# Kernel optimization log

Measured on AMD Instinct MI355X. Metric: run time of the kernel, lower is better.

## Reference

```python
import jax, jax.numpy as jnp
import numpy as np

D_MODEL = 512
NHEAD = 8
HEAD_DIM = D_MODEL // NHEAD
NS = 1  # num_special_tokens


def setup_inputs() -> dict:
    key = jax.random.key(0)
    ks = jax.random.split(key, 12)
    B, N = 8, 1024
    x = jax.random.normal(ks[0], (B, N, D_MODEL), dtype=jnp.float32)
    coords = jax.random.normal(ks[1], (B, N, 3), dtype=jnp.float32) * 5.0
    key_padding_mask = jnp.zeros((B, N), dtype=bool)
    s = 1.0 / np.sqrt(D_MODEL)
    qkv_w = jax.random.normal(ks[2], (3 * D_MODEL, D_MODEL), dtype=jnp.float32) * s
    out_w = jax.random.normal(ks[3], (D_MODEL, D_MODEL), dtype=jnp.float32) * s
    out_b = jnp.zeros((D_MODEL,), dtype=jnp.float32)
    bias_alpha = jnp.ones((1,), dtype=jnp.float32) * 0.5  # nonzero so bias path matters
    w1 = jax.random.normal(ks[4], (NHEAD * 4, 4), dtype=jnp.float32) * 0.5
    b1 = jnp.zeros((NHEAD * 4,), dtype=jnp.float32)
    w2 = jax.random.normal(ks[5], (NHEAD, NHEAD * 4), dtype=jnp.float32) * 0.2
    b2 = jnp.zeros((NHEAD,), dtype=jnp.float32)
    coord_scales = jnp.array([12.0, 12.0, 5.0], dtype=jnp.float32)
    return dict(x=x, coords=coords, key_padding_mask=key_padding_mask,
                qkv_w=qkv_w, out_w=out_w, out_b=out_b, bias_alpha=bias_alpha,
                w1=w1, b1=b1, w2=w2, b2=b2, coord_scales=coord_scales)


def reference(x, coords, key_padding_mask, qkv_w, out_w, out_b, bias_alpha,
              w1, b1, w2, b2, coord_scales):
    B, N, _ = x.shape
    scale = HEAD_DIM ** (-0.5)
    qkv = x @ qkv_w.T  # [B,N,3D]
    q, k, v = jnp.split(qkv, 3, axis=-1)
    def heads(t):
        return t.reshape(B, N, NHEAD, HEAD_DIM).transpose(0, 2, 1, 3)  # [B,H,N,dh]
    q, k, v = heads(q), heads(k), heads(v)

    c = coords / coord_scales  # [B,N,3]
    dpos = c[:, :, None, :] - c[:, None, :, :]  # [B,N,N,3]
    dist = jnp.linalg.norm(dpos, axis=-1, keepdims=True)  # [B,N,N,1]
    feat = jnp.concatenate([dpos, dist], axis=-1)  # [B,N,N,4]
    h = jax.nn.gelu(feat @ w1.T + b1, approximate=False)  # [B,N,N,4H]
    bias = (h @ w2.T + b2).transpose(0, 3, 1, 2)  # [B,H,N,N]
    # zero out bias rows/cols for special tokens
    bias = bias.at[:, :, :NS, :].set(0.0)
    bias = bias.at[:, :, :, :NS].set(0.0)

    dots = jnp.einsum('bhid,bhjd->bhij', q, k) * scale
    logits = dots + bias_alpha * bias
    logits = jnp.where(key_padding_mask[:, None, None, :], -1e30, logits)
    attn = jax.nn.softmax(logits, axis=-1)
    out = jnp.einsum('bhij,bhjd->bhid', attn, v)
    out = out.transpose(0, 2, 1, 3).reshape(B, N, D_MODEL)
    return out @ out_w.T + out_b
```

## Files before the change

### kernel.cpp

```cpp
#include <hip/hip_runtime.h>
#include <hip/hip_bf16.h>
#include <math.h>

#define D_MODEL 512
#define NHEAD   8
#define HEAD_DIM 64
#define BB      8
#define NN      1024
#define NS      1
#define TI      16
#define TJ      32
#define NT      (NN / TJ)
#define FIX_M   10.0f
#define GSTRIDE 40

typedef __attribute__((ext_vector_type(8))) short short8;
typedef __attribute__((ext_vector_type(4))) float floatx4;

__device__ __forceinline__ float gelu_tanh(float x) {
    const float x2 = x * x;
    const float z  = x * fmaf(0.0713548162f, x2, 1.5957691216f);
    const float e  = __expf(z);
    const float r  = __builtin_amdgcn_rcpf(1.0f + e);
    return fmaf(-x, r, x);
}

__device__ __forceinline__ unsigned short f2bf(float f) {
    unsigned u = __float_as_uint(f);
    u = (u + 0x7fffu + ((u >> 16) & 1u)) >> 16;
    return (unsigned short)u;
}

__device__ __forceinline__ uint2 pack4bf(float a, float b, float c, float d) {
    uint2 p;
    p.x = (unsigned)f2bf(a) | ((unsigned)f2bf(b) << 16);
    p.y = (unsigned)f2bf(c) | ((unsigned)f2bf(d) << 16);
    return p;
}

__global__ __launch_bounds__(256)
void gemm_qkv_mfma(const float* __restrict__ A, const float* __restrict__ Bm,
                   unsigned short* __restrict__ Qb, unsigned short* __restrict__ Kb,
                   unsigned short* __restrict__ Vt) {
    __shared__ __align__(16) unsigned short As[128 * GSTRIDE];
    __shared__ __align__(16) unsigned short Bs[128 * GSTRIDE];
    const int tid = threadIdx.x;
    const int bm = blockIdx.y * 128;
    const int bn = blockIdx.x * 128;
    const int wv = tid >> 6, lane = tid & 63, quad = lane >> 4, ln = lane & 15;
    const int wm = (wv >> 1) * 64, wn = (wv & 1) * 64;

    floatx4 acc[4][4];
    #pragma unroll
    for (int i = 0; i < 4; ++i)
        #pragma unroll
        for (int j = 0; j < 4; ++j) acc[i][j] = (floatx4){0.f, 0.f, 0.f, 0.f};

    for (int k0 = 0; k0 < 512; k0 += 32) {
        __syncthreads();
        #pragma unroll
        for (int t = 0; t < 4; ++t) {
            const int c = tid + t * 256;
            const int row = c >> 3, kc = (c & 7) * 4;
            float4 v = *(const float4*)(A + (size_t)(bm + row) * 512 + k0 + kc);
            *(uint2*)&As[row * GSTRIDE + kc] = pack4bf(v.x, v.y, v.z, v.w);
            float4 w = *(const float4*)(Bm + (size_t)(bn + row) * 512 + k0 + kc);
            *(uint2*)&Bs[row * GSTRIDE + kc] = pack4bf(w.x, w.y, w.z, w.w);
        }
        __syncthreads();
        short8 af[4], bf[4];
        #pragma unroll
        for (int mb = 0; mb < 4; ++mb)
            af[mb] = *(const short8*)&As[(wm + mb * 16 + ln) * GSTRIDE + quad * 8];
        #pragma unroll
        for (int nb = 0; nb < 4; ++nb)
            bf[nb] = *(const short8*)&Bs[(wn + nb * 16 + ln) * GSTRIDE + quad * 8];
        #pragma unroll
        for (int mb = 0; mb < 4; ++mb)
            #pragma unroll
            for (int nb = 0; nb < 4; ++nb)
                acc[mb][nb] = __builtin_amdgcn_mfma_f32_16x16x32_bf16(af[mb], bf[nb], acc[mb][nb], 0, 0, 0);
    }

    #pragma unroll
    for (int nb = 0; nb < 4; ++nb) {
        const int n = bn + wn + nb * 16 + ln;
        #pragma unroll
        for (int mb = 0; mb < 4; ++mb) {
            const int m = bm + wm + mb * 16 + quad * 4;
            if (n < 512) {
                #pragma unroll
                for (int r = 0; r < 4; ++r)
                    Qb[(size_t)(m + r) * 512 + n] = f2bf(acc[mb][nb][r] * 0.125f);
            } else if (n < 1024) {
                #pragma unroll
                for (int r = 0; r < 4; ++r)
                    Kb[(size_t)(m + r) * 512 + (n - 512)] = f2bf(acc[mb][nb][r]);
            } else {
                const int bb = m >> 10, tok = m & 1023;
                *(uint2*)(Vt + ((size_t)bb * 512 + (n - 1024)) * NN + tok) =
                    pack4bf(acc[mb][nb][0], acc[mb][nb][1], acc[mb][nb][2], acc[mb][nb][3]);
            }
        }
    }
}

__global__ __launch_bounds__(256)
void gemm_out_mfma(const unsigned short* __restrict__ Ab, const float* __restrict__ Bm,
                   const float* __restrict__ bias, float* __restrict__ C) {
    __shared__ __align__(16) unsigned short As[128 * GSTRIDE];
    __shared__ __align__(16) unsigned short Bs[128 * GSTRIDE];
    const int tid = threadIdx.x;
    const int bm = blockIdx.y * 128;
    const int bn = blockIdx.x * 128;
    const int wv = tid >> 6, lane = tid & 63, quad = lane >> 4, ln = lane & 15;
    const int wm = (wv >> 1) * 64, wn = (wv & 1) * 64;

    floatx4 acc[4][4];
    #pragma unroll
    for (int i = 0; i < 4; ++i)
        #pragma unroll
        for (int j = 0; j < 4; ++j) acc[i][j] = (floatx4){0.f, 0.f, 0.f, 0.f};

    for (int k0 = 0; k0 < 512; k0 += 32) {
        __syncthreads();
        #pragma unroll
        for (int t = 0; t < 4; ++t) {
            const int c = tid + t * 256;
            const int row = c >> 3, kc = (c & 7) * 4;
            *(uint2*)&As[row * GSTRIDE + kc] =
                *(const uint2*)(Ab + (size_t)(bm + row) * 512 + k0 + kc);
            float4 w = *(const float4*)(Bm + (size_t)(bn + row) * 512 + k0 + kc);
            *(uint2*)&Bs[row * GSTRIDE + kc] = pack4bf(w.x, w.y, w.z, w.w);
        }
        __syncthreads();
        short8 af[4], bf[4];
        #pragma unroll
        for (int mb = 0; mb < 4; ++mb)
            af[mb] = *(const short8*)&As[(wm + mb * 16 + ln) * GSTRIDE + quad * 8];
        #pragma unroll
        for (int nb = 0; nb < 4; ++nb)
            bf[nb] = *(const short8*)&Bs[(wn + nb * 16 + ln) * GSTRIDE + quad * 8];
        #pragma unroll
        for (int mb = 0; mb < 4; ++mb)
            #pragma unroll
            for (int nb = 0; nb < 4; ++nb)
                acc[mb][nb] = __builtin_amdgcn_mfma_f32_16x16x32_bf16(af[mb], bf[nb], acc[mb][nb], 0, 0, 0);
    }

    #pragma unroll
    for (int nb = 0; nb < 4; ++nb) {
        const int n = bn + wn + nb * 16 + ln;
        const float bv = bias[n];
        #pragma unroll
        for (int mb = 0; mb < 4; ++mb) {
            const int m = bm + wm + mb * 16 + quad * 4;
            #pragma unroll
            for (int r = 0; r < 4; ++r)
                C[(size_t)(m + r) * 512 + n] = acc[mb][nb][r] + bv;
        }
    }
}

#define BIAS_IDX(i, j, h) ((i) * 291 + (j) * 9 + (h))
__global__ __launch_bounds__(256, 2)
void attn_kernel(const unsigned short* __restrict__ Qb,
                 const unsigned short* __restrict__ Kb,
                 const unsigned short* __restrict__ Vt,
                 const float* __restrict__ coords,
                 const unsigned char* __restrict__ mask,
                 const float* __restrict__ w1, const float* __restrict__ b1,
                 const float* __restrict__ w2, const float* __restrict__ b2,
                 const float* __restrict__ coord_scales,
                 const float* __restrict__ alpha_p,
                 unsigned short* __restrict__ attn_out) {
    const int b   = blockIdx.y;
    const int i0  = blockIdx.x * TI;
    const int tid = threadIdx.x;
    const int wv  = tid >> 6;
    const int lane = tid & 63;
    const int quad = lane >> 4;
    const int ln   = lane & 15;
    const int h0   = wv * 2;

    __shared__ float bias_s[2][TI * 291 + 9];
    __shared__ __align__(16) unsigned short ps[NHEAD][TI][40];

    const float alpha = alpha_p[0];
    const float isx = 1.0f / coord_scales[0];
    const float isy = 1.0f / coord_scales[1];
    const float isz = 1.0f / coord_scales[2];

    float cir[4][3];
    #pragma unroll
    for (int g = 0; g < 4; ++g) {
        const float* cp = coords + ((size_t)b * NN + i0 + wv * 4 + g) * 3;
        cir[g][0] = cp[0] * isx; cir[g][1] = cp[1] * isy; cir[g][2] = cp[2] * isz;
    }

    float4 w1r[8]; float b1r[8];
    #pragma unroll
    for (int jj = 0; jj < 8; ++jj) {
        w1r[jj] = *(const float4*)(w1 + (quad * 8 + jj) * 4);
        b1r[jj] = b1[quad * 8 + jj];
    }
    short8 b2f;
    #pragma unroll
    for (int jj = 0; jj < 8; ++jj) {
        const float v = (ln < 8) ? alpha * w2[ln * 32 + quad * 8 + jj] : 0.0f;
        b2f[jj] = (short)f2bf(v);
    }
    const float ab2 = (ln < 8) ? alpha * b2[ln] : 0.0f;

    short8 qf[2][2];
    #pragma unroll
    for (int hh = 0; hh < 2; ++hh)
        #pragma unroll
        for (int kd = 0; kd < 2; ++kd)
            qf[hh][kd] = *(const short8*)(Qb + ((size_t)b * NN + i0 + ln) * 512
                                          + (h0 + hh) * 64 + kd * 32 + quad * 8);

    floatx4 oacc[2][4];
    #pragma unroll
    for (int hh = 0; hh < 2; ++hh)
        #pragma unroll
        for (int nd = 0; nd < 4; ++nd)
            oacc[hh][nd] = (floatx4){0.f, 0.f, 0.f, 0.f};
    float l_part[2][4];
    #pragma unroll
    for (int hh = 0; hh < 2; ++hh)
        #pragma unroll
        for (int r = 0; r < 4; ++r) l_part[hh][r] = 0.f;

    const unsigned char* maskp = mask + (size_t)b * NN;
    float cjx[2], cjy[2], cjz[2];

    #define LOAD_CJ(tt_) do { const int tt = (tt_);                               \
        if (tt < NT) {                                                            \
            const float* cp0 = coords + ((size_t)b * NN + tt * TJ + ln) * 3;      \
            cjx[0] = cp0[0] * isx; cjy[0] = cp0[1] * isy; cjz[0] = cp0[2] * isz;  \
            cjx[1] = cp0[48] * isx; cjy[1] = cp0[49] * isy; cjz[1] = cp0[50] * isz; \
        } } while (0)

    #define MLP_TILE(tt_) do { const int tt = (tt_);                              \
        if (tt < NT) {                                                            \
            float* bout = bias_s[tt & 1];                                         \
            const int j0m = tt * TJ;                                              \
            _Pragma("unroll")                                                     \
            for (int g = 0; g < 4; ++g) {                                         \
                const int i = wv * 4 + g;                                         \
                const float cix = cir[g][0], ciy = cir[g][1], ciz = cir[g][2];    \
                const bool irow0 = (i0 + i < NS);                                 \
                _Pragma("unroll")                                                 \
                for (int jh = 0; jh < 2; ++jh) {                                  \
                    const float dx = cix - cjx[jh];                               \
                    const float dy = ciy - cjy[jh];                               \
                    const float dz = ciz - cjz[jh];                               \
                    const float dist = sqrtf(dx * dx + dy * dy + dz * dz);        \
                    float hu[8];                                                  \
                    _Pragma("unroll")                                             \
                    for (int jj = 0; jj < 8; ++jj) {                              \
                        const float4 wa = w1r[jj];                                \
                        float t0 = fmaf(wa.x, dx, fmaf(wa.y, dy,                  \
                                   fmaf(wa.z, dz, fmaf(wa.w, dist, b1r[jj]))));   \
                        hu[jj] = gelu_tanh(t0);                                   \
                    }                                                             \
                    union { short8 s8; unsigned u4[4]; } H;                       \
                    _Pragma("unroll")                                             \
                    for (int k = 0; k < 4; ++k) {                                 \
                        __hip_bfloat162 t2 = __float22bfloat162_rn(               \
                            make_float2(hu[2 * k], hu[2 * k + 1]));               \
                        H.u4[k] = *(unsigned*)&t2;                                \
                    }                                                             \
                    floatx4 D = __builtin_amdgcn_mfma_f32_16x16x32_bf16(          \
                        H.s8, b2f, (floatx4){0.f, 0.f, 0.f, 0.f}, 0, 0, 0);       \
                    if (ln < 8) {                                                 \
                        _Pragma("unroll")                                         \
                        for (int r = 0; r < 4; ++r) {                             \
                            const int jw = jh * 16 + quad * 4 + r;                \
                            const float val = (irow0 || (j0m + jw < NS))          \
                                              ? 0.0f : (D[r] + ab2);              \
                            bout[BIAS_IDX(i, jw, ln)] = val;                      \
                        }                                                         \
                    }                                                             \
                }                                                                 \
            }                                                                     \
        } } while (0)

    LOAD_CJ(0);
    MLP_TILE(0);
    __syncthreads();

    for (int jt = 0; jt < NT; ++jt) {
        const int j0 = jt * TJ;
        const int pb = jt & 1;

        short8 kf[2][4], vf[2][4];
        #pragma unroll
        for (int hh = 0; hh < 2; ++hh) {
            const unsigned short* kbase = Kb + ((size_t)b * NN + j0) * 512 + (h0 + hh) * 64;
            kf[hh][0] = *(const short8*)(kbase + (size_t)ln * 512 + quad * 8);
            kf[hh][1] = *(const short8*)(kbase + (size_t)ln * 512 + 32 + quad * 8);
            kf[hh][2] = *(const short8*)(kbase + (size_t)(16 + ln) * 512 + quad * 8);
            kf[hh][3] = *(const short8*)(kbase + (size_t)(16 + ln) * 512 + 32 + quad * 8);
            const unsigned short* vbase = Vt + ((size_t)b * 512 + (h0 + hh) * 64) * NN + j0 + quad * 8;
            #pragma unroll
            for (int nd = 0; nd < 4; ++nd)
                vf[hh][nd] = *(const short8*)(vbase + (size_t)(nd * 16 + ln) * NN);
        }
        const unsigned char mm0 = maskp[j0 + ln];
        const unsigned char mm1 = maskp[j0 + 16 + ln];

        LOAD_CJ(jt + 1);
        MLP_TILE(jt + 1);

        #pragma unroll
        for (int hh = 0; hh < 2; ++hh) {
            const int h = h0 + hh;
            floatx4 s0 = (floatx4){0.f, 0.f, 0.f, 0.f};
            floatx4 s1 = (floatx4){0.f, 0.f, 0.f, 0.f};
            s0 = __builtin_amdgcn_mfma_f32_16x16x32_bf16(qf[hh][0], kf[hh][0], s0, 0, 0, 0);
            s0 = __builtin_amdgcn_mfma_f32_16x16x32_bf16(qf[hh][1], kf[hh][1], s0, 0, 0, 0);
            s1 = __builtin_amdgcn_mfma_f32_16x16x32_bf16(qf[hh][0], kf[hh][2], s1, 0, 0, 0);
            s1 = __builtin_amdgcn_mfma_f32_16x16x32_bf16(qf[hh][1], kf[hh][3], s1, 0, 0, 0);
            #pragma unroll
            for (int r = 0; r < 4; ++r) {
                const int row = quad * 4 + r;
                float v0 = s0[r] + bias_s[pb][BIAS_IDX(row, ln, h)];
                float v1 = s1[r] + bias_s[pb][BIAS_IDX(row, 16 + ln, h)];
                v0 = mm0 ? -1e30f : v0;
                v1 = mm1 ? -1e30f : v1;
                const float e0 = __expf(v0 - FIX_M);
                const float e1 = __expf(v1 - FIX_M);
                l_part[hh][r] += e0 + e1;
                ps[h][row][ln]      = f2bf(e0);
                ps[h][row][16 + ln] = f2bf(e1);
            }
        }

        asm volatile("s_waitcnt lgkmcnt(0)" ::: "memory");

        #pragma unroll
        for (int hh = 0; hh < 2; ++hh) {
            const int h = h0 + hh;
            short8 pa = *(const short8*)&ps[h][ln][quad * 8];
            #pragma unroll
            for (int nd = 0; nd < 4; ++nd)
                oacc[hh][nd] = __builtin_amdgcn_mfma_f32_16x16x32_bf16(pa, vf[hh][nd], oacc[hh][nd], 0, 0, 0);
        }

        __syncthreads();
    }

    #pragma unroll
    for (int hh = 0; hh < 2; ++hh) {
        float rl[4];
        #pragma unroll
        for (int r = 0; r < 4; ++r) {
            float l = l_part[hh][r];
            l += __shfl_xor(l, 1, 64);
            l += __shfl_xor(l, 2, 64);
            l += __shfl_xor(l, 4, 64);
            l += __shfl_xor(l, 8, 64);
            rl[r] = 1.0f / l;
        }
        #pragma unroll
        for (int nd = 0; nd < 4; ++nd)
            #pragma unroll
            for (int r = 0; r < 4; ++r)
                attn_out[((size_t)b * NN + i0 + quad * 4 + r) * 512
                         + (h0 + hh) * 64 + nd * 16 + ln] = f2bf(oacc[hh][nd][r] * rl[r]);
    }
    #undef LOAD_CJ
    #undef MLP_TILE
}

extern "C" void kernel_launch(void* const* d_in, const int* in_sizes, int n_in,
                              void* d_out, int out_size, void* d_ws, size_t ws_size,
                              hipStream_t stream) {
    const float* x        = (const float*)d_in[0];
    const float* coords   = (const float*)d_in[1];
    const unsigned char* kpm = (const unsigned char*)d_in[2];
    const float* qkv_w    = (const float*)d_in[3];
    const float* out_w    = (const float*)d_in[4];
    const float* out_b    = (const float*)d_in[5];
    const float* alpha    = (const float*)d_in[6];
    const float* w1       = (const float*)d_in[7];
    const float* b1       = (const float*)d_in[8];
    const float* w2       = (const float*)d_in[9];
    const float* b2       = (const float*)d_in[10];
    const float* cscales  = (const float*)d_in[11];
    float* out = (float*)d_out;

    const int M = BB * NN;
    unsigned short* Qb = (unsigned short*)d_ws;
    unsigned short* Kb = Qb + (size_t)M * D_MODEL;
    unsigned short* Vt = Kb + (size_t)M * D_MODEL;
    unsigned short* Ao = Vt + (size_t)M * D_MODEL;

    {
        dim3 grid(3 * D_MODEL / 128, M / 128);
        gemm_qkv_mfma<<<grid, 256, 0, stream>>>(x, qkv_w, Qb, Kb, Vt);
    }
    {
        dim3 grid(NN / TI, BB);
        attn_kernel<<<grid, 256, 0, stream>>>(Qb, Kb, Vt, coords, kpm, w1, b1, w2, b2,
                                              cscales, alpha, Ao);
    }
    {
        dim3 grid(D_MODEL / 128, M / 128);
        gemm_out_mfma<<<grid, 256, 0, stream>>>(Ao, out_w, out_b, out);
    }
}
```

Measured before the change: 360.5 us.

## Split attention key range across two wave groups and store bias in fp16

```diff
diff --git a/kernel.cpp b/kernel.cpp
--- a/kernel.cpp
+++ b/kernel.cpp
@@ -11,6 +11,7 @@
 #define TI      16
 #define TJ      32
 #define NT      (NN / TJ)
+#define NTH     (NT / 2)
 #define FIX_M   10.0f
 #define GSTRIDE 40
 
@@ -163,7 +164,10 @@
 }
 
 #define BIAS_IDX(i, j, h) ((i) * 291 + (j) * 9 + (h))
-__global__ __launch_bounds__(256, 2)
+#define BIAS_HALVES (TI * 291 + 9)
+#define PS_OFF   37376
+#define SMEM_SZ  (PS_OFF + 2 * NHEAD * 16 * 40 * 2)
+__global__ __launch_bounds__(512, 2)
 void attn_kernel(const unsigned short* __restrict__ Qb,
                  const unsigned short* __restrict__ Kb,
                  const unsigned short* __restrict__ Vt,
@@ -178,13 +182,17 @@
     const int i0  = blockIdx.x * TI;
     const int tid = threadIdx.x;
     const int wv  = tid >> 6;
+    const int g2  = wv >> 2;
+    const int wq  = wv & 3;
     const int lane = tid & 63;
     const int quad = lane >> 4;
     const int ln   = lane & 15;
-    const int h0   = wv * 2;
-
-    __shared__ float bias_s[2][TI * 291 + 9];
-    __shared__ __align__(16) unsigned short ps[NHEAD][TI][40];
+    const int h0   = wq * 2;
+
+    __shared__ __align__(16) unsigned char smem[SMEM_SZ];
+    _Float16 (*bias_s)[BIAS_HALVES] = (_Float16 (*)[BIAS_HALVES])smem;
+    unsigned short (*psg)[16][40] =
+        (unsigned short (*)[16][40])(smem + PS_OFF + g2 * (NHEAD * 16 * 40 * 2));
 
     const float alpha = alpha_p[0];
     const float isx = 1.0f / coord_scales[0];
@@ -194,7 +202,7 @@
     float cir[4][3];
     #pragma unroll
     for (int g = 0; g < 4; ++g) {
-        const float* cp = coords + ((size_t)b * NN + i0 + wv * 4 + g) * 3;
+        const float* cp = coords + ((size_t)b * NN + i0 + wq * 4 + g) * 3;
         cir[g][0] = cp[0] * isx; cir[g][1] = cp[1] * isy; cir[g][2] = cp[2] * isz;
     }
 
@@ -235,20 +243,23 @@
     const unsigned char* maskp = mask + (size_t)b * NN;
     float cjx[2], cjy[2], cjz[2];
 
+    const int t0   = g2 * NTH;
+    const int tEnd = t0 + NTH;
+
     #define LOAD_CJ(tt_) do { const int tt = (tt_);                               \
-        if (tt < NT) {                                                            \
+        if (tt < tEnd) {                                                          \
             const float* cp0 = coords + ((size_t)b * NN + tt * TJ + ln) * 3;      \
             cjx[0] = cp0[0] * isx; cjy[0] = cp0[1] * isy; cjz[0] = cp0[2] * isz;  \
             cjx[1] = cp0[48] * isx; cjy[1] = cp0[49] * isy; cjz[1] = cp0[50] * isz; \
         } } while (0)
 
     #define MLP_TILE(tt_) do { const int tt = (tt_);                              \
-        if (tt < NT) {                                                            \
-            float* bout = bias_s[tt & 1];                                         \
+        if (tt < tEnd) {                                                          \
+            _Float16* bout = bias_s[g2 * 2 + (tt & 1)];                           \
             const int j0m = tt * TJ;                                              \
             _Pragma("unroll")                                                     \
             for (int g = 0; g < 4; ++g) {                                         \
-                const int i = wv * 4 + g;                                         \
+                const int i = wq * 4 + g;                                         \
                 const float cix = cir[g][0], ciy = cir[g][1], ciz = cir[g][2];    \
                 const bool irow0 = (i0 + i < NS);                                 \
                 _Pragma("unroll")                                                 \
@@ -261,9 +272,9 @@
                     _Pragma("unroll")                                             \
                     for (int jj = 0; jj < 8; ++jj) {                              \
                         const float4 wa = w1r[jj];                                \
-                        float t0 = fmaf(wa.x, dx, fmaf(wa.y, dy,                  \
-                                   fmaf(wa.z, dz, fmaf(wa.w, dist, b1r[jj]))));   \
-                        hu[jj] = gelu_tanh(t0);                                   \
+                        float t0v = fmaf(wa.x, dx, fmaf(wa.y, dy,                 \
+                                    fmaf(wa.z, dz, fmaf(wa.w, dist, b1r[jj]))));  \
+                        hu[jj] = gelu_tanh(t0v);                                  \
                     }                                                             \
                     union { short8 s8; unsigned u4[4]; } H;                       \
                     _Pragma("unroll")                                             \
@@ -280,20 +291,20 @@
                             const int jw = jh * 16 + quad * 4 + r;                \
                             const float val = (irow0 || (j0m + jw < NS))          \
                                               ? 0.0f : (D[r] + ab2);              \
-                            bout[BIAS_IDX(i, jw, ln)] = val;                      \
+                            bout[BIAS_IDX(i, jw, ln)] = (_Float16)val;            \
                         }                                                         \
                     }                                                             \
                 }                                                                 \
             }                                                                     \
         } } while (0)
 
-    LOAD_CJ(0);
-    MLP_TILE(0);
+    LOAD_CJ(t0);
+    MLP_TILE(t0);
     __syncthreads();
 
-    for (int jt = 0; jt < NT; ++jt) {
+    for (int jt = t0; jt < tEnd; ++jt) {
         const int j0 = jt * TJ;
-        const int pb = jt & 1;
+        const _Float16* bp = bias_s[g2 * 2 + (jt & 1)];
 
         short8 kf[2][4], vf[2][4];
         #pragma unroll
@@ -326,24 +337,26 @@
             #pragma unroll
             for (int r = 0; r < 4; ++r) {
                 const int row = quad * 4 + r;
-                float v0 = s0[r] + bias_s[pb][BIAS_IDX(row, ln, h)];
-                float v1 = s1[r] + bias_s[pb][BIAS_IDX(row, 16 + ln, h)];
+                float v0 = s0[r] + (float)bp[BIAS_IDX(row, ln, h)];
+                float v1 = s1[r] + (float)bp[BIAS_IDX(row, 16 + ln, h)];
                 v0 = mm0 ? -1e30f : v0;
                 v1 = mm1 ? -1e30f : v1;
                 const float e0 = __expf(v0 - FIX_M);
                 const float e1 = __expf(v1 - FIX_M);
                 l_part[hh][r] += e0 + e1;
-                ps[h][row][ln]      = f2bf(e0);
-                ps[h][row][16 + ln] = f2bf(e1);
+                psg[h][row][ln]      = f2bf(e0);
+                psg[h][row][16 + ln] = f2bf(e1);
             }
         }
 
+        __builtin_amdgcn_sched_barrier(0);
         asm volatile("s_waitcnt lgkmcnt(0)" ::: "memory");
+        __builtin_amdgcn_sched_barrier(0);
 
         #pragma unroll
         for (int hh = 0; hh < 2; ++hh) {
             const int h = h0 + hh;
-            short8 pa = *(const short8*)&ps[h][ln][quad * 8];
+            short8 pa = *(const short8*)&psg[h][ln][quad * 8];
             #pragma unroll
             for (int nd = 0; nd < 4; ++nd)
                 oacc[hh][nd] = __builtin_amdgcn_mfma_f32_16x16x32_bf16(pa, vf[hh][nd], oacc[hh][nd], 0, 0, 0);
@@ -352,9 +365,9 @@
         __syncthreads();
     }
 
-    #pragma unroll
-    for (int hh = 0; hh < 2; ++hh) {
-        float rl[4];
+    float lsum[2][4];
+    #pragma unroll
+    for (int hh = 0; hh < 2; ++hh)
         #pragma unroll
         for (int r = 0; r < 4; ++r) {
             float l = l_part[hh][r];
@@ -362,14 +375,47 @@
             l += __shfl_xor(l, 2, 64);
             l += __shfl_xor(l, 4, 64);
             l += __shfl_xor(l, 8, 64);
-            rl[r] = 1.0f / l;
-        }
-        #pragma unroll
-        for (int nd = 0; nd < 4; ++nd)
+            lsum[hh][r] = l;
+        }
+
+    __syncthreads();
+    float* Olds = (float*)smem;
+    float* Llds = (float*)(smem + 32768);
+    if (g2 == 1) {
+        #pragma unroll
+        for (int hh = 0; hh < 2; ++hh) {
+            const int h = h0 + hh;
+            #pragma unroll
+            for (int nd = 0; nd < 4; ++nd)
+                #pragma unroll
+                for (int r = 0; r < 4; ++r)
+                    Olds[((h * 16) + quad * 4 + r) * 64 + nd * 16 + ln] = oacc[hh][nd][r];
+            if (ln == 0) {
+                #pragma unroll
+                for (int r = 0; r < 4; ++r)
+                    Llds[h * 16 + quad * 4 + r] = lsum[hh][r];
+            }
+        }
+    }
+    __syncthreads();
+    if (g2 == 0) {
+        #pragma unroll
+        for (int hh = 0; hh < 2; ++hh) {
+            const int h = h0 + hh;
+            float rl[4];
             #pragma unroll
             for (int r = 0; r < 4; ++r)
-                attn_out[((size_t)b * NN + i0 + quad * 4 + r) * 512
-                         + (h0 + hh) * 64 + nd * 16 + ln] = f2bf(oacc[hh][nd][r] * rl[r]);
+                rl[r] = 1.0f / (lsum[hh][r] + Llds[h * 16 + quad * 4 + r]);
+            #pragma unroll
+            for (int nd = 0; nd < 4; ++nd)
+                #pragma unroll
+                for (int r = 0; r < 4; ++r) {
+                    const float o = oacc[hh][nd][r]
+                                  + Olds[((h * 16) + quad * 4 + r) * 64 + nd * 16 + ln];
+                    attn_out[((size_t)b * NN + i0 + quad * 4 + r) * 512
+                             + h * 64 + nd * 16 + ln] = f2bf(o * rl[r]);
+                }
+        }
     }
     #undef LOAD_CJ
     #undef MLP_TILE
@@ -404,7 +450,7 @@
     }
     {
         dim3 grid(NN / TI, BB);
-        attn_kernel<<<grid, 256, 0, stream>>>(Qb, Kb, Vt, coords, kpm, w1, b1, w2, b2,
+        attn_kernel<<<grid, 512, 0, stream>>>(Qb, Kb, Vt, coords, kpm, w1, b1, w2, b2,
                                               cscales, alpha, Ao);
     }
     {
```

Measured after the change: 410.0 us. +13.7%, slower.
